# Kernel tuning notes

Hardware: AMD Instinct MI355X
Metric: run time of the kernel (lower is better)

## Reference

```python
import jax, jax.numpy as jnp
import numpy as np

B, NPG, H, D = 8, 6250, 4, 128   # graphs, nodes/graph, heads, hidden
N = B * NPG                       # 50000 nodes total
E = 400000                        # edges
VOCAB = 10000


def setup_inputs() -> dict:
    key = jax.random.key(0)
    ks = jax.random.split(key, 12)
    p = lambda k, shape: jax.random.normal(k, shape, dtype=jnp.float32) * 0.05
    return {
        "node_ids": jax.random.randint(ks[0], (N,), 0, VOCAB),
        "src": jax.random.randint(ks[1], (E,), 0, N),
        "dst": jax.random.randint(ks[2], (E,), 0, N),
        "emb": p(ks[3], (VOCAB, D)),
        "W_src": p(ks[4], (D, H * D)), "b_src": jnp.zeros((H * D,), jnp.float32),
        "W_dst": p(ks[5], (D, H * D)), "b_dst": jnp.zeros((H * D,), jnp.float32),
        "attn": p(ks[6], (H, D)),
        "W_res": p(ks[7], (D, H * D)), "b_res": jnp.zeros((H * D,), jnp.float32),
        "W_gc": p(ks[8], (D, D)), "b_gc": jnp.zeros((D,), jnp.float32),
        "W_mlp": p(ks[9], (3 * D, 1)), "b_mlp": jnp.zeros((1,), jnp.float32),
    }


def _leaky(x, s):
    return jnp.where(x >= 0, x, s * x)


def _maxpool(feat):
    # dgl.max_nodes: per-graph max over nodes -> [B, feat_dim]
    return jnp.max(feat.reshape(B, NPG, -1), axis=1)


def _gatv2(x, src, dst, W_src, b_src, W_dst, b_dst, attn, W_res, b_res):
    # DGL GATv2Conv (share_weights=False, residual=True, eval mode -> no dropout)
    hs = (x @ W_src + b_src).reshape(N, H, D)
    hd = (x @ W_dst + b_dst).reshape(N, H, D)
    e = _leaky(hs[src] + hd[dst], 0.2)              # [E,H,D]
    logits = jnp.einsum('ehd,hd->eh', e, attn)      # [E,H]
    m = jax.ops.segment_max(logits, dst, num_segments=N)
    ex = jnp.exp(logits - m[dst])
    denom = jax.ops.segment_sum(ex, dst, num_segments=N)
    alpha = ex / denom[dst]                          # edge softmax per dst/head
    rst = jax.ops.segment_sum(hs[src] * alpha[..., None], dst, num_segments=N)
    rst = rst + (x @ W_res + b_res).reshape(N, H, D)
    return _leaky(rst, 0.01)                         # nn.LeakyReLU() activation


def _graphconv(x, src, dst, W, b):
    # DGL GraphConv norm='both', allow_zero_in_degree=True, LeakyReLU activation
    ones = jnp.ones((E,), x.dtype)
    dout = jnp.clip(jax.ops.segment_sum(ones, src, num_segments=N), 1.0, None)
    din = jnp.clip(jax.ops.segment_sum(ones, dst, num_segments=N), 1.0, None)
    h = x * jax.lax.rsqrt(dout)[:, None]
    agg = jax.ops.segment_sum(h[src], dst, num_segments=N)
    h = agg * jax.lax.rsqrt(din)[:, None]
    return _leaky(h @ W + b, 0.01)


def reference(node_ids, src, dst, emb, W_src, b_src, W_dst, b_dst, attn,
              W_res, b_res, W_gc, b_gc, W_mlp, b_mlp):
    feat = emb[node_ids]                             # featurize_nodes
    pools = [_maxpool(feat)]
    res = _gatv2(feat, src, dst, W_src, b_src, W_dst, b_dst, attn,
                 W_res, b_res).mean(axis=1)          # mean over heads -> [N,D]
    pools.append(_maxpool(res))
    res = _graphconv(res, src, dst, W_gc, b_gc)
    pools.append(_maxpool(res))
    agg = jnp.concatenate(pools, axis=1)             # [B, 3D]
    # reward_predictor_block_two: ReLU -> (Dropout eval) -> Linear(3D, 1)
    return jax.nn.relu(agg) @ W_mlp + b_mlp          # BCE logits [B,1]
```

## Files before the change

### kernel.cpp

```cpp
#include <hip/hip_runtime.h>
#include <float.h>
#include <math.h>

#define Bg   8
#define NPGc 6250
#define Hh   4
#define Dd   128
#define Nn   50000
#define Ee   400000
#define HDd  512
#define NCHUNK 49

typedef unsigned short ushort_t;
typedef __attribute__((ext_vector_type(8))) short bf16x8;
typedef __attribute__((ext_vector_type(4))) float f32x4;
typedef __attribute__((ext_vector_type(2))) float f32x2;

__device__ __forceinline__ void atomicMaxF(float* addr, float val) {
    if (val >= 0.0f) atomicMax((int*)addr, __float_as_int(val));
    else             atomicMin((unsigned int*)addr, __float_as_uint(val));
}

__device__ __forceinline__ ushort_t f2bf(float x) {
    unsigned u = __float_as_uint(x);
    unsigned r = (u + 0x7FFFu + ((u >> 16) & 1u)) >> 16;
    return (ushort_t)r;
}

__device__ __forceinline__ f32x2 bfpair(unsigned u) {
    f32x2 r;
    r.x = __uint_as_float(u << 16);
    r.y = __uint_as_float(u & 0xFFFF0000u);
    return r;
}

__global__ void setup_kernel(const int* __restrict__ ids, const float* __restrict__ emb,
                             ushort_t* __restrict__ feat_bf,
                             const float* __restrict__ W_src, const float* __restrict__ W_dst,
                             const float* __restrict__ W_res, const float* __restrict__ W_gc,
                             const float* __restrict__ b_src, const float* __restrict__ b_dst,
                             const float* __restrict__ b_res,
                             ushort_t* __restrict__ Wt_s, ushort_t* __restrict__ Wt_dr,
                             ushort_t* __restrict__ Wt_gc,
                             float* __restrict__ bias_s, float* __restrict__ bias_dr,
                             int* __restrict__ din_i, float* __restrict__ dout,
                             int* __restrict__ cursor, float* __restrict__ pools) {
    int i = blockIdx.x * blockDim.x + threadIdx.x;
    {
        int n = i >> 5, c = i & 31;
        int id = ids[n];
        float4 v = ((const float4*)emb)[(size_t)id * 32 + c];
        ushort4 b;
        b.x = f2bf(v.x); b.y = f2bf(v.y); b.z = f2bf(v.z); b.w = f2bf(v.w);
        ((ushort4*)feat_bf)[(size_t)n * 32 + c] = b;
    }
    if (i < Nn) { din_i[i] = 0; dout[i] = 0.0f; cursor[i] = 0; }
    if (i < Bg * 3 * Dd) pools[i] = -FLT_MAX;
    if (i < 512 * 128) {
        int c = i >> 7, k = i & 127;
        Wt_s[i] = f2bf(W_src[k * 512 + c]);
    } else if (i < 512 * 128 + 1024 * 128) {
        int j = i - 512 * 128;
        int c = j >> 7, k = j & 127;
        float v = (c < 512) ? W_dst[k * 512 + c] : W_res[k * 512 + (c - 512)];
        Wt_dr[j] = f2bf(v);
    } else if (i < 512 * 128 + 1024 * 128 + 128 * 128) {
        int j = i - (512 * 128 + 1024 * 128);
        int c = j >> 7, k = j & 127;
        Wt_gc[j] = f2bf(W_gc[k * 128 + c]);
    }
    if (i < 512) bias_s[i] = b_src[i];
    if (i < 1024) bias_dr[i] = (i < 512) ? b_dst[i] : b_res[i - 512];
}

__global__ void maxpool_bf_kernel(const ushort_t* __restrict__ x, float* __restrict__ pools, int col_off) {
    int b = blockIdx.x, chunk = blockIdx.y, lane = threadIdx.x;
    int i0 = chunk * 125;
    f32x2 mx = {-FLT_MAX, -FLT_MAX};
    for (int i = 0; i < 125; ++i) {
        unsigned u = *(const unsigned*)(x + ((size_t)(b * NPGc + i0 + i)) * Dd + lane * 2);
        mx = __builtin_elementwise_max(mx, bfpair(u));
    }
    atomicMaxF(&pools[b * (3 * Dd) + col_off + lane * 2],     mx.x);
    atomicMaxF(&pools[b * (3 * Dd) + col_off + lane * 2 + 1], mx.y);
}

template<int GNT, int NCS>
__global__ __launch_bounds__(256) void mfma_gemm_kernel(
    const ushort_t* __restrict__ A, const ushort_t* __restrict__ Wt,
    const float* __restrict__ bias, ushort_t* __restrict__ Ob,
    int n_rows, int WN)
{
    __shared__ ushort_t Cs[2][64 * 64];
    int bid = blockIdx.x;
    int lin = (bid & 7) * (gridDim.x >> 3) + (bid >> 3);
    int row0 = (lin / NCS) * 64;
    int ct0  = (lin % NCS) * GNT;
    int w = threadIdx.x >> 6, lane = threadIdx.x & 63;
    int lrow = lane & 15, kg = lane >> 4;

    bf16x8 av[4][4];
    {
        const ushort_t* ap = A + (size_t)(row0 + lrow) * 128 + kg * 8;
        #pragma unroll
        for (int fi = 0; fi < 4; ++fi)
            #pragma unroll
            for (int ks = 0; ks < 4; ++ks)
                av[fi][ks] = *(const bf16x8*)(ap + fi * 16 * 128 + ks * 32);
    }
    bf16x8 wv[GNT][4];
    float4 bv[GNT];
    {
        const ushort_t* wp = Wt + (size_t)(ct0 * 64 + w * 16 + lrow) * 128 + kg * 8;
        #pragma unroll
        for (int ct = 0; ct < GNT; ++ct) {
            #pragma unroll
            for (int ks = 0; ks < 4; ++ks)
                wv[ct][ks] = *(const bf16x8*)(wp + (size_t)ct * 8192 + ks * 32);
            bv[ct] = *(const float4*)(bias + (ct0 + ct) * 64 + w * 16 + kg * 4);
        }
    }

    #pragma unroll
    for (int ct = 0; ct < GNT; ++ct) {
        f32x4 acc[4] = {};
        #pragma unroll
        for (int ks = 0; ks < 4; ++ks)
            #pragma unroll
            for (int fi = 0; fi < 4; ++fi)
                acc[fi] = __builtin_amdgcn_mfma_f32_16x16x32_bf16(wv[ct][ks], av[fi][ks], acc[fi], 0, 0, 0);

        ushort_t* cb = Cs[ct & 1];
        int cbase = w * 32 + kg * 8;
        #pragma unroll
        for (int fi = 0; fi < 4; ++fi) {
            float o0 = acc[fi][0] + bv[ct].x;
            float o1 = acc[fi][1] + bv[ct].y;
            float o2 = acc[fi][2] + bv[ct].z;
            float o3 = acc[fi][3] + bv[ct].w;
            unsigned q0, q1;
            asm("v_cvt_pk_bf16_f32 %0, %1, %2" : "=v"(q0) : "v"(o0), "v"(o1));
            asm("v_cvt_pk_bf16_f32 %0, %1, %2" : "=v"(q1) : "v"(o2), "v"(o3));
            int r = fi * 16 + lrow;
            int cbyte = cbase ^ ((r & 7) << 4);
            uint2 q; q.x = q0; q.y = q1;
            *(uint2*)((char*)cb + r * 128 + cbyte) = q;
        }
        __syncthreads();
        {
            int t = threadIdx.x;
            const char* cbr = (const char*)cb;
            #pragma unroll
            for (int h = 0; h < 2; ++h) {
                int r  = (h * 256 + t) >> 3;
                int ch = t & 7;
                int cbyte = (ch * 16) ^ ((r & 7) << 4);
                uint4 v = *(const uint4*)(cbr + r * 128 + cbyte);
                int grow = row0 + r;
                if (grow < n_rows)
                    *(uint4*)((char*)Ob + ((size_t)grow * WN + (ct0 + ct) * 64) * 2 + ch * 16) = v;
            }
        }
    }
}

__global__ __launch_bounds__(256) void mfma_gc_pool_kernel(
    const ushort_t* __restrict__ A, const ushort_t* __restrict__ Wt,
    const float* __restrict__ bias, float* __restrict__ pools)
{
    int g = blockIdx.x / 98, lb = blockIdx.x % 98;
    int row0 = g * NPGc + lb * 64;
    int w = threadIdx.x >> 6, lane = threadIdx.x & 63;
    int lrow = lane & 15, kg = lane >> 4;

    bf16x8 av[4][4];
    {
        const ushort_t* ap = A + (size_t)(row0 + lrow) * 128 + kg * 8;
        #pragma unroll
        for (int fi = 0; fi < 4; ++fi)
            #pragma unroll
            for (int ks = 0; ks < 4; ++ks)
                av[fi][ks] = *(const bf16x8*)(ap + fi * 16 * 128 + ks * 32);
    }

    #pragma unroll
    for (int ct = 0; ct < 2; ++ct) {
        bf16x8 wv[4];
        const ushort_t* wp = Wt + (size_t)(ct * 64 + w * 16 + lrow) * 128 + kg * 8;
        #pragma unroll
        for (int ks = 0; ks < 4; ++ks) wv[ks] = *(const bf16x8*)(wp + ks * 32);

        f32x4 acc[4] = {};
        #pragma unroll
        for (int ks = 0; ks < 4; ++ks)
            #pragma unroll
            for (int fi = 0; fi < 4; ++fi)
                acc[fi] = __builtin_amdgcn_mfma_f32_16x16x32_bf16(wv[ks], av[fi][ks], acc[fi], 0, 0, 0);

        int colb = ct * 64 + w * 16 + kg * 4;
        float4 bv4 = *(const float4*)(bias + colb);
        float mcol[4] = {-FLT_MAX, -FLT_MAX, -FLT_MAX, -FLT_MAX};
        #pragma unroll
        for (int fi = 0; fi < 4; ++fi) {
            int lr = lb * 64 + fi * 16 + lrow;
            bool valid = lr < NPGc;
            #pragma unroll
            for (int j = 0; j < 4; ++j) {
                float v = acc[fi][j] + ((const float*)&bv4)[j];
                v = v >= 0.0f ? v : 0.01f * v;
                if (valid) mcol[j] = fmaxf(mcol[j], v);
            }
        }
        #pragma unroll
        for (int j = 0; j < 4; ++j) {
            mcol[j] = fmaxf(mcol[j], __shfl_xor(mcol[j], 1));
            mcol[j] = fmaxf(mcol[j], __shfl_xor(mcol[j], 2));
            mcol[j] = fmaxf(mcol[j], __shfl_xor(mcol[j], 4));
            mcol[j] = fmaxf(mcol[j], __shfl_xor(mcol[j], 8));
        }
        if (lrow == 0) {
            #pragma unroll
            for (int j = 0; j < 4; ++j)
                atomicMaxF(&pools[g * (3 * Dd) + 2 * Dd + colb + j], mcol[j]);
        }
    }
}

__global__ void degree2_kernel(const int* __restrict__ src, const int* __restrict__ dst,
                               int* __restrict__ din_i, float* __restrict__ dout) {
    int e = blockIdx.x * blockDim.x + threadIdx.x;
    if (e >= Ee) return;
    atomicAdd(&din_i[dst[e]], 1);
    atomicAdd(&dout[src[e]], 1.0f);
}

__global__ __launch_bounds__(256) void scan_reduce_kernel(const int* __restrict__ din_i,
                                                          int* __restrict__ partials) {
    int b = blockIdx.x, t = threadIdx.x;
    int base = b * 1024 + t * 4;
    int s = 0;
    #pragma unroll
    for (int j = 0; j < 4; ++j) { int i = base + j; if (i < Nn) s += din_i[i]; }
    #pragma unroll
    for (int off = 32; off > 0; off >>= 1) s += __shfl_xor(s, off);
    __shared__ int wsum[4];
    if ((t & 63) == 0) wsum[t >> 6] = s;
    __syncthreads();
    if (t == 0) partials[b] = wsum[0] + wsum[1] + wsum[2] + wsum[3];
}

__global__ void scan_mid_kernel(int* __restrict__ partials, int* __restrict__ row_start) {
    if (threadIdx.x == 0) {
        int acc = 0;
        for (int i = 0; i < NCHUNK; ++i) { int v = partials[i]; partials[i] = acc; acc += v; }
        row_start[Nn] = acc;
    }
}

__global__ __launch_bounds__(256) void scan_final_kernel(const int* __restrict__ din_i,
                                                         const int* __restrict__ partials,
                                                         int* __restrict__ row_start,
                                                         float* __restrict__ din_f) {
    int b = blockIdx.x, t = threadIdx.x;
    int base = b * 1024 + t * 4;
    int v[4]; int s = 0;
    #pragma unroll
    for (int j = 0; j < 4; ++j) {
        v[j] = (base + j < Nn) ? din_i[base + j] : 0;
        s += v[j];
    }
    __shared__ int buf[256];
    buf[t] = s;
    __syncthreads();
    #pragma unroll
    for (int off = 1; off < 256; off <<= 1) {
        int x = (t >= off) ? buf[t - off] : 0;
        __syncthreads();
        buf[t] += x;
        __syncthreads();
    }
    int excl = buf[t] - s + partials[b];
    #pragma unroll
    for (int j = 0; j < 4; ++j) {
        if (base + j < Nn) {
            row_start[base + j] = excl;
            din_f[base + j] = (float)v[j];
            excl += v[j];
        }
    }
}

__global__ void scatter_kernel(const int* __restrict__ src, const int* __restrict__ dst,
                               const int* __restrict__ row_start, int* __restrict__ cursor,
                               int* __restrict__ csr_src) {
    int e = blockIdx.x * blockDim.x + threadIdx.x;
    if (e >= Ee) return;
    int d = dst[e];
    int slot = row_start[d] + atomicAdd(&cursor[d], 1);
    csr_src[slot] = src[e];
}

__global__ __launch_bounds__(256) void gat_fused_kernel(
    const ushort_t* __restrict__ hs, const ushort_t* __restrict__ hdres,
    const float* __restrict__ attn,
    const int* __restrict__ row_start, const int* __restrict__ csr_src,
    ushort_t* __restrict__ res_bf)
{
    int d = (blockIdx.x * 256 + threadIdx.x) >> 6;
    int lane = threadIdx.x & 63;
    if (d >= Nn) return;
    int e0 = row_start[d], e1 = row_start[d + 1];

    const f32x2 z2 = {0.0f, 0.0f};
    f32x2 hd0, hd1, hd2, hd3, at0, at1, at2, at3;
    {
        uint4 hr = *(const uint4*)(hdres + (size_t)d * 1024 + lane * 8);
        hd0 = bfpair(hr.x); hd1 = bfpair(hr.y); hd2 = bfpair(hr.z); hd3 = bfpair(hr.w);
        float4 a0 = *(const float4*)(attn + lane * 8);
        float4 a1 = *(const float4*)(attn + lane * 8 + 4);
        at0.x = a0.x; at0.y = a0.y; at1.x = a0.z; at1.y = a0.w;
        at2.x = a1.x; at2.y = a1.y; at3.x = a1.z; at3.y = a1.w;
    }

    float denom = 0.0f;
    f32x2 ac0 = z2, ac1 = z2, ac2 = z2, ac3 = z2;

#define LOGIT_PRE(rr, h0, h1, h2, h3, pout)                                           \
    {                                                                                 \
        h0 = bfpair(rr.x); h1 = bfpair(rr.y); h2 = bfpair(rr.z); h3 = bfpair(rr.w);   \
        f32x2 p2 = z2;                                                                \
        { f32x2 x = h0 + hd0;                                                         \
          p2 += (__builtin_elementwise_max(x, z2) + 0.2f * __builtin_elementwise_min(x, z2)) * at0; } \
        { f32x2 x = h1 + hd1;                                                         \
          p2 += (__builtin_elementwise_max(x, z2) + 0.2f * __builtin_elementwise_min(x, z2)) * at1; } \
        { f32x2 x = h2 + hd2;                                                         \
          p2 += (__builtin_elementwise_max(x, z2) + 0.2f * __builtin_elementwise_min(x, z2)) * at2; } \
        { f32x2 x = h3 + hd3;                                                         \
          p2 += (__builtin_elementwise_max(x, z2) + 0.2f * __builtin_elementwise_min(x, z2)) * at3; } \
        pout = p2.x + p2.y;                                                           \
    }

    int e = e0;
    for (; e + 4 <= e1; e += 4) {
        int sA = csr_src[e], sB = csr_src[e + 1], sC = csr_src[e + 2], sD = csr_src[e + 3];
        uint4 rA = *(const uint4*)(hs + (size_t)sA * HDd + lane * 8);
        uint4 rB = *(const uint4*)(hs + (size_t)sB * HDd + lane * 8);
        uint4 rC = *(const uint4*)(hs + (size_t)sC * HDd + lane * 8);
        uint4 rD = *(const uint4*)(hs + (size_t)sD * HDd + lane * 8);
        f32x2 hA0, hA1, hA2, hA3, hB0, hB1, hB2, hB3;
        f32x2 hC0, hC1, hC2, hC3, hD0, hD1, hD2, hD3;
        float pA, pB, pC, pD;
        LOGIT_PRE(rA, hA0, hA1, hA2, hA3, pA);
        LOGIT_PRE(rB, hB0, hB1, hB2, hB3, pB);
        LOGIT_PRE(rC, hC0, hC1, hC2, hC3, pC);
        LOGIT_PRE(rD, hD0, hD1, hD2, hD3, pD);
        pA += __shfl_xor(pA, 1); pB += __shfl_xor(pB, 1); pC += __shfl_xor(pC, 1); pD += __shfl_xor(pD, 1);
        pA += __shfl_xor(pA, 2); pB += __shfl_xor(pB, 2); pC += __shfl_xor(pC, 2); pD += __shfl_xor(pD, 2);
        pA += __shfl_xor(pA, 4); pB += __shfl_xor(pB, 4); pC += __shfl_xor(pC, 4); pD += __shfl_xor(pD, 4);
        pA += __shfl_xor(pA, 8); pB += __shfl_xor(pB, 8); pC += __shfl_xor(pC, 8); pD += __shfl_xor(pD, 8);
        float exA = __expf(fminf(fmaxf(pA, -40.0f), 40.0f));
        float exB = __expf(fminf(fmaxf(pB, -40.0f), 40.0f));
        float exC = __expf(fminf(fmaxf(pC, -40.0f), 40.0f));
        float exD = __expf(fminf(fmaxf(pD, -40.0f), 40.0f));
        denom += (exA + exB) + (exC + exD);
        ac0 += hA0 * exA + hB0 * exB + hC0 * exC + hD0 * exD;
        ac1 += hA1 * exA + hB1 * exB + hC1 * exC + hD1 * exD;
        ac2 += hA2 * exA + hB2 * exB + hC2 * exC + hD2 * exD;
        ac3 += hA3 * exA + hB3 * exB + hC3 * exC + hD3 * exD;
    }
    for (; e < e1; ++e) {
        int s = csr_src[e];
        uint4 rr = *(const uint4*)(hs + (size_t)s * HDd + lane * 8);
        f32x2 h0, h1, h2, h3;
        float p;
        LOGIT_PRE(rr, h0, h1, h2, h3, p);
        p += __shfl_xor(p, 1); p += __shfl_xor(p, 2);
        p += __shfl_xor(p, 4); p += __shfl_xor(p, 8);
        float ex = __expf(fminf(fmaxf(p, -40.0f), 40.0f));
        denom += ex;
        ac0 += h0 * ex; ac1 += h1 * ex; ac2 += h2 * ex; ac3 += h3 * ex;
    }
#undef LOGIT_PRE

    float inv = (e1 > e0) ? 1.0f / denom : 0.0f;
    f32x2 rv0, rv1, rv2, rv3;
    {
        uint4 rr = *(const uint4*)(hdres + (size_t)d * 1024 + 512 + lane * 8);
        rv0 = bfpair(rr.x); rv1 = bfpair(rr.y); rv2 = bfpair(rr.z); rv3 = bfpair(rr.w);
    }
    float t[8];
    {
        f32x2 v0 = ac0 * inv + rv0, v1 = ac1 * inv + rv1;
        f32x2 v2 = ac2 * inv + rv2, v3 = ac3 * inv + rv3;
        f32x2 l0 = __builtin_elementwise_max(v0, z2) + 0.01f * __builtin_elementwise_min(v0, z2);
        f32x2 l1 = __builtin_elementwise_max(v1, z2) + 0.01f * __builtin_elementwise_min(v1, z2);
        f32x2 l2 = __builtin_elementwise_max(v2, z2) + 0.01f * __builtin_elementwise_min(v2, z2);
        f32x2 l3 = __builtin_elementwise_max(v3, z2) + 0.01f * __builtin_elementwise_min(v3, z2);
        t[0] = l0.x; t[1] = l0.y; t[2] = l1.x; t[3] = l1.y;
        t[4] = l2.x; t[5] = l2.y; t[6] = l3.x; t[7] = l3.y;
    }
    #pragma unroll
    for (int j = 0; j < 8; ++j) {
        t[j] += __shfl_xor(t[j], 16);
        t[j] += __shfl_xor(t[j], 32);
    }
    if (lane < 16) {
        float o0 = 0.25f * t[0], o1 = 0.25f * t[1], o2 = 0.25f * t[2], o3 = 0.25f * t[3];
        float o4 = 0.25f * t[4], o5 = 0.25f * t[5], o6 = 0.25f * t[6], o7 = 0.25f * t[7];
        unsigned q0, q1, q2, q3;
        asm("v_cvt_pk_bf16_f32 %0, %1, %2" : "=v"(q0) : "v"(o0), "v"(o1));
        asm("v_cvt_pk_bf16_f32 %0, %1, %2" : "=v"(q1) : "v"(o2), "v"(o3));
        asm("v_cvt_pk_bf16_f32 %0, %1, %2" : "=v"(q2) : "v"(o4), "v"(o5));
        asm("v_cvt_pk_bf16_f32 %0, %1, %2" : "=v"(q3) : "v"(o6), "v"(o7));
        uint4 qb; qb.x = q0; qb.y = q1; qb.z = q2; qb.w = q3;
        *(uint4*)(res_bf + (size_t)d * Dd + lane * 8) = qb;
    }
}

__global__ __launch_bounds__(256) void gc_gather_kernel(
    const ushort_t* __restrict__ res_bf, const int* __restrict__ row_start,
    const int* __restrict__ csr_src, const float* __restrict__ dout,
    const float* __restrict__ din, ushort_t* __restrict__ agg_bf)
{
    int d = (blockIdx.x * 256 + threadIdx.x) >> 6;
    int lane = threadIdx.x & 63;
    if (d >= Nn) return;
    int e0 = row_start[d], e1 = row_start[d + 1];
    const f32x2 z2 = {0.0f, 0.0f};
    f32x2 a2 = z2;
    int s0 = (e0 < e1) ? csr_src[e0] : 0;
    int s1 = (e0 + 1 < e1) ? csr_src[e0 + 1] : s0;
    float sc0 = 1.0f / sqrtf(fmaxf((e0 < e1) ? dout[s0] : 1.0f, 1.0f));
    float sc1 = 1.0f / sqrtf(fmaxf((e0 + 1 < e1) ? dout[s1] : 1.0f, 1.0f));
    unsigned u0 = *(const unsigned*)(res_bf + (size_t)s0 * Dd + lane * 2);
    unsigned u1 = *(const unsigned*)(res_bf + (size_t)s1 * Dd + lane * 2);
    for (int e = e0; e < e1; ++e) {
        int s2 = (e + 2 < e1) ? csr_src[e + 2] : s0;
        float sc2 = 1.0f / sqrtf(fmaxf(dout[s2], 1.0f));
        unsigned u2 = *(const unsigned*)(res_bf + (size_t)s2 * Dd + lane * 2);
        a2 += bfpair(u0) * sc0;
        u0 = u1; u1 = u2; sc0 = sc1; sc1 = sc2;
    }
    float scd = 1.0f / sqrtf(fmaxf(din[d], 1.0f));
    float ax = a2.x * scd, ay = a2.y * scd;
    unsigned q;
    asm("v_cvt_pk_bf16_f32 %0, %1, %2" : "=v"(q) : "v"(ax), "v"(ay));
    *(unsigned*)(agg_bf + (size_t)d * Dd + lane * 2) = q;
}

__global__ void final_kernel(const float* __restrict__ pools, const float* __restrict__ W_mlp,
                             const float* __restrict__ b_mlp, float* __restrict__ out) {
    int b = blockIdx.x, lane = threadIdx.x;
    float s = 0.0f;
    for (int j = lane; j < 3 * Dd; j += 64)
        s += fmaxf(pools[b * (3 * Dd) + j], 0.0f) * W_mlp[j];
    #pragma unroll
    for (int off = 32; off > 0; off >>= 1) s += __shfl_xor(s, off);
    if (lane == 0) out[b] = s + b_mlp[0];
}

extern "C" void kernel_launch(void* const* d_in, const int* in_sizes, int n_in,
                              void* d_out, int out_size, void* d_ws, size_t ws_size,
                              hipStream_t stream) {
    const int*   node_ids = (const int*)d_in[0];
    const int*   src      = (const int*)d_in[1];
    const int*   dst      = (const int*)d_in[2];
    const float* emb      = (const float*)d_in[3];
    const float* W_src    = (const float*)d_in[4];
    const float* b_src    = (const float*)d_in[5];
    const float* W_dst    = (const float*)d_in[6];
    const float* b_dst    = (const float*)d_in[7];
    const float* attn     = (const float*)d_in[8];
    const float* W_res    = (const float*)d_in[9];
    const float* b_res    = (const float*)d_in[10];
    const float* W_gc     = (const float*)d_in[11];
    const float* b_gc     = (const float*)d_in[12];
    const float* W_mlp    = (const float*)d_in[13];
    const float* b_mlp    = (const float*)d_in[14];
    float* out = (float*)d_out;

    char* w = (char*)d_ws;
    size_t off = 0;
    ushort_t* feat_bf = (ushort_t*)(w + off); off += (size_t)(Nn + 64) * Dd * 2;
    ushort_t* hs_buf  = (ushort_t*)(w + off); off += (size_t)Nn * HDd * 2;
    ushort_t* hdres   = (ushort_t*)(w + off); off += (size_t)Nn * 1024 * 2;
    ushort_t* Wt_s    = (ushort_t*)(w + off); off += (size_t)512 * 128 * 2;
    ushort_t* Wt_dr   = (ushort_t*)(w + off); off += (size_t)1024 * 128 * 2;
    ushort_t* Wt_gc   = (ushort_t*)(w + off); off += (size_t)128 * 128 * 2;
    float*    bias_s  = (float*)(w + off);    off += 512 * 4;
    float*    bias_dr = (float*)(w + off);    off += 1024 * 4;
    int*      csr_src = (int*)(w + off);      off += (size_t)Ee * 4;
    int*      row_st  = (int*)(w + off);      off += ((size_t)Nn + 4) * 4;
    int*      cursor  = (int*)(w + off);      off += (size_t)Nn * 4;
    int*      din_i   = (int*)(w + off);      off += (size_t)Nn * 4;
    float*    din_f   = (float*)(w + off);    off += (size_t)Nn * 4;
    float*    dout_f  = (float*)(w + off);    off += (size_t)Nn * 4;
    int*      partials= (int*)(w + off);      off += 64 * 4;
    float*    pools   = (float*)(w + off);    off += (size_t)Bg * 3 * Dd * 4;
    ushort_t* res_bf  = (ushort_t*)(w + off); off += (size_t)Nn * Dd * 2;

    ushort_t* agg_bf = hs_buf;

    setup_kernel<<<(Nn * 32) / 256, 256, 0, stream>>>(
        node_ids, emb, feat_bf, W_src, W_dst, W_res, W_gc,
        b_src, b_dst, b_res, Wt_s, Wt_dr, Wt_gc, bias_s, bias_dr,
        din_i, dout_f, cursor, pools);
    maxpool_bf_kernel<<<dim3(Bg, 50), 64, 0, stream>>>(feat_bf, pools, 0);

    degree2_kernel<<<(Ee + 255) / 256, 256, 0, stream>>>(src, dst, din_i, dout_f);
    scan_reduce_kernel<<<NCHUNK, 256, 0, stream>>>(din_i, partials);
    scan_mid_kernel<<<1, 64, 0, stream>>>(partials, row_st);
    scan_final_kernel<<<NCHUNK, 256, 0, stream>>>(din_i, partials, row_st, din_f);
    scatter_kernel<<<(Ee + 255) / 256, 256, 0, stream>>>(src, dst, row_st, cursor, csr_src);

    mfma_gemm_kernel<2, 4><<<((Nn + 63) / 64) * 4, 256, 0, stream>>>(
        feat_bf, Wt_s, bias_s, hs_buf, Nn, HDd);
    mfma_gemm_kernel<2, 8><<<((Nn + 63) / 64) * 8, 256, 0, stream>>>(
        feat_bf, Wt_dr, bias_dr, hdres, Nn, 1024);

    gat_fused_kernel<<<(Nn * 64) / 256, 256, 0, stream>>>(
        hs_buf, hdres, attn, row_st, csr_src, res_bf);
    maxpool_bf_kernel<<<dim3(Bg, 50), 64, 0, stream>>>(res_bf, pools, Dd);

    gc_gather_kernel<<<(Nn * 64) / 256, 256, 0, stream>>>(res_bf, row_st, csr_src, dout_f, din_f, agg_bf);
    mfma_gc_pool_kernel<<<Bg * 98, 256, 0, stream>>>(agg_bf, Wt_gc, b_gc, pools);

    final_kernel<<<Bg, 64, 0, stream>>>(pools, W_mlp, b_mlp, out);
}
```

Measured before the change: 384.4 us.

## Merge src/dst/res GEMMs into one launch and use nontemporal hdres traffic

```diff
diff --git a/kernel.cpp b/kernel.cpp
--- a/kernel.cpp
+++ b/kernel.cpp
@@ -9,12 +9,14 @@
 #define Nn   50000
 #define Ee   400000
 #define HDd  512
+#define WNf  1536
 #define NCHUNK 49
 
 typedef unsigned short ushort_t;
 typedef __attribute__((ext_vector_type(8))) short bf16x8;
 typedef __attribute__((ext_vector_type(4))) float f32x4;
 typedef __attribute__((ext_vector_type(2))) float f32x2;
+typedef __attribute__((ext_vector_type(4))) unsigned u32x4;
 
 __device__ __forceinline__ void atomicMaxF(float* addr, float val) {
     if (val >= 0.0f) atomicMax((int*)addr, __float_as_int(val));
@@ -40,9 +42,8 @@
                              const float* __restrict__ W_res, const float* __restrict__ W_gc,
                              const float* __restrict__ b_src, const float* __restrict__ b_dst,
                              const float* __restrict__ b_res,
-                             ushort_t* __restrict__ Wt_s, ushort_t* __restrict__ Wt_dr,
-                             ushort_t* __restrict__ Wt_gc,
-                             float* __restrict__ bias_s, float* __restrict__ bias_dr,
+                             ushort_t* __restrict__ Wt, ushort_t* __restrict__ Wt_gc,
+                             float* __restrict__ bias_f,
                              int* __restrict__ din_i, float* __restrict__ dout,
                              int* __restrict__ cursor, float* __restrict__ pools) {
     int i = blockIdx.x * blockDim.x + threadIdx.x;
@@ -56,21 +57,19 @@
     }
     if (i < Nn) { din_i[i] = 0; dout[i] = 0.0f; cursor[i] = 0; }
     if (i < Bg * 3 * Dd) pools[i] = -FLT_MAX;
-    if (i < 512 * 128) {
+    if (i < WNf * 128) {
         int c = i >> 7, k = i & 127;
-        Wt_s[i] = f2bf(W_src[k * 512 + c]);
-    } else if (i < 512 * 128 + 1024 * 128) {
-        int j = i - 512 * 128;
-        int c = j >> 7, k = j & 127;
-        float v = (c < 512) ? W_dst[k * 512 + c] : W_res[k * 512 + (c - 512)];
-        Wt_dr[j] = f2bf(v);
-    } else if (i < 512 * 128 + 1024 * 128 + 128 * 128) {
-        int j = i - (512 * 128 + 1024 * 128);
+        float v = (c < 512) ? W_src[k * 512 + c]
+                : (c < 1024) ? W_dst[k * 512 + (c - 512)]
+                             : W_res[k * 512 + (c - 1024)];
+        Wt[i] = f2bf(v);
+    } else if (i < WNf * 128 + 128 * 128) {
+        int j = i - WNf * 128;
         int c = j >> 7, k = j & 127;
         Wt_gc[j] = f2bf(W_gc[k * 128 + c]);
     }
-    if (i < 512) bias_s[i] = b_src[i];
-    if (i < 1024) bias_dr[i] = (i < 512) ? b_dst[i] : b_res[i - 512];
+    if (i < WNf)
+        bias_f[i] = (i < 512) ? b_src[i] : (i < 1024) ? b_dst[i - 512] : b_res[i - 1024];
 }
 
 __global__ void maxpool_bf_kernel(const ushort_t* __restrict__ x, float* __restrict__ pools, int col_off) {
@@ -85,11 +84,12 @@
     atomicMaxF(&pools[b * (3 * Dd) + col_off + lane * 2 + 1], mx.y);
 }
 
-template<int GNT, int NCS>
+#define GNT 2
+#define NCS 12
 __global__ __launch_bounds__(256) void mfma_gemm_kernel(
     const ushort_t* __restrict__ A, const ushort_t* __restrict__ Wt,
-    const float* __restrict__ bias, ushort_t* __restrict__ Ob,
-    int n_rows, int WN)
+    const float* __restrict__ bias, ushort_t* __restrict__ Ohs,
+    ushort_t* __restrict__ Odr, int n_rows)
 {
     __shared__ ushort_t Cs[2][64 * 64];
     int bid = blockIdx.x;
@@ -150,15 +150,22 @@
         {
             int t = threadIdx.x;
             const char* cbr = (const char*)cb;
+            int gcol = (ct0 + ct) * 64;
+            char* ob; int wn;
+            if (gcol < 512) { ob = (char*)Ohs; wn = 512; }
+            else            { ob = (char*)Odr; wn = 1024; gcol -= 512; }
             #pragma unroll
             for (int h = 0; h < 2; ++h) {
                 int r  = (h * 256 + t) >> 3;
                 int ch = t & 7;
                 int cbyte = (ch * 16) ^ ((r & 7) << 4);
-                uint4 v = *(const uint4*)(cbr + r * 128 + cbyte);
+                u32x4 v = *(const u32x4*)(cbr + r * 128 + cbyte);
                 int grow = row0 + r;
-                if (grow < n_rows)
-                    *(uint4*)((char*)Ob + ((size_t)grow * WN + (ct0 + ct) * 64) * 2 + ch * 16) = v;
+                if (grow < n_rows) {
+                    u32x4* dp = (u32x4*)(ob + ((size_t)grow * wn + gcol) * 2 + ch * 16);
+                    if (wn == 1024) __builtin_nontemporal_store(v, dp);
+                    else            *dp = v;
+                }
             }
         }
     }
@@ -314,7 +321,7 @@
     const f32x2 z2 = {0.0f, 0.0f};
     f32x2 hd0, hd1, hd2, hd3, at0, at1, at2, at3;
     {
-        uint4 hr = *(const uint4*)(hdres + (size_t)d * 1024 + lane * 8);
+        u32x4 hr = __builtin_nontemporal_load((const u32x4*)(hdres + (size_t)d * 1024 + lane * 8));
         hd0 = bfpair(hr.x); hd1 = bfpair(hr.y); hd2 = bfpair(hr.z); hd3 = bfpair(hr.w);
         float4 a0 = *(const float4*)(attn + lane * 8);
         float4 a1 = *(const float4*)(attn + lane * 8 + 4);
@@ -385,7 +392,7 @@
     float inv = (e1 > e0) ? 1.0f / denom : 0.0f;
     f32x2 rv0, rv1, rv2, rv3;
     {
-        uint4 rr = *(const uint4*)(hdres + (size_t)d * 1024 + 512 + lane * 8);
+        u32x4 rr = __builtin_nontemporal_load((const u32x4*)(hdres + (size_t)d * 1024 + 512 + lane * 8));
         rv0 = bfpair(rr.x); rv1 = bfpair(rr.y); rv2 = bfpair(rr.z); rv3 = bfpair(rr.w);
     }
     float t[8];
@@ -484,11 +491,9 @@
     ushort_t* feat_bf = (ushort_t*)(w + off); off += (size_t)(Nn + 64) * Dd * 2;
     ushort_t* hs_buf  = (ushort_t*)(w + off); off += (size_t)Nn * HDd * 2;
     ushort_t* hdres   = (ushort_t*)(w + off); off += (size_t)Nn * 1024 * 2;
-    ushort_t* Wt_s    = (ushort_t*)(w + off); off += (size_t)512 * 128 * 2;
-    ushort_t* Wt_dr   = (ushort_t*)(w + off); off += (size_t)1024 * 128 * 2;
+    ushort_t* Wt      = (ushort_t*)(w + off); off += (size_t)WNf * 128 * 2;
     ushort_t* Wt_gc   = (ushort_t*)(w + off); off += (size_t)128 * 128 * 2;
-    float*    bias_s  = (float*)(w + off);    off += 512 * 4;
-    float*    bias_dr = (float*)(w + off);    off += 1024 * 4;
+    float*    bias_f  = (float*)(w + off);    off += (size_t)WNf * 4;
     int*      csr_src = (int*)(w + off);      off += (size_t)Ee * 4;
     int*      row_st  = (int*)(w + off);      off += ((size_t)Nn + 4) * 4;
     int*      cursor  = (int*)(w + off);      off += (size_t)Nn * 4;
@@ -503,7 +508,7 @@
 
     setup_kernel<<<(Nn * 32) / 256, 256, 0, stream>>>(
         node_ids, emb, feat_bf, W_src, W_dst, W_res, W_gc,
-        b_src, b_dst, b_res, Wt_s, Wt_dr, Wt_gc, bias_s, bias_dr,
+        b_src, b_dst, b_res, Wt, Wt_gc, bias_f,
         din_i, dout_f, cursor, pools);
     maxpool_bf_kernel<<<dim3(Bg, 50), 64, 0, stream>>>(feat_bf, pools, 0);
 
@@ -513,10 +518,8 @@
     scan_final_kernel<<<NCHUNK, 256, 0, stream>>>(din_i, partials, row_st, din_f);
     scatter_kernel<<<(Ee + 255) / 256, 256, 0, stream>>>(src, dst, row_st, cursor, csr_src);
 
-    mfma_gemm_kernel<2, 4><<<((Nn + 63) / 64) * 4, 256, 0, stream>>>(
-        feat_bf, Wt_s, bias_s, hs_buf, Nn, HDd);
-    mfma_gemm_kernel<2, 8><<<((Nn + 63) / 64) * 8, 256, 0, stream>>>(
-        feat_bf, Wt_dr, bias_dr, hdres, Nn, 1024);
+    mfma_gemm_kernel<<<((Nn + 63) / 64) * NCS, 256, 0, stream>>>(
+        feat_bf, Wt, bias_f, hs_buf, hdres, Nn);
 
     gat_fused_kernel<<<(Nn * 64) / 256, 256, 0, stream>>>(
         hs_buf, hdres, attn, row_st, csr_src, res_bf);
```

New measurement: 377.8 us. Within noise of the previous version (-1.7%).
